# Kernel tuning notes

Measured on AMD Instinct MI355X. Metric: run time of the kernel, lower is better.

The kernel has to match this reference:

```python
import jax, jax.numpy as jnp
import numpy as np

IMAGE_SIZE = 256
NEAR = 0.1
FAR = 100.0
EPS = 1e-3
BACKGROUND = (0.0, 0.0, 0.0)
CHUNK = 64   # faces per scan step (bounds peak memory of the z-buffer pass)
TINY = 1e-12


def _bary(vx, vy, vz, xp, yp):
    """Barycentric weights / perspective-correct depth at pixel centers.
    vx, vy, vz: 3-tuples of vertex coords, broadcastable with xp/yp.
    Mirrors the CUDA kernel: unnormalized cross-product weights, normalize,
    clamp to [0,1], renormalize, zp = 1 / sum(w_k / z_k), near/far clip."""
    x0, x1, x2 = vx; y0, y1, y2 = vy; z0, z1, z2 = vz
    w0 = yp * (x2 - x1) + xp * (y1 - y2) + (x1 * y2 - x2 * y1)
    w1 = yp * (x0 - x2) + xp * (y2 - y0) + (x2 * y0 - x0 * y2)
    w2 = yp * (x1 - x0) + xp * (y0 - y1) + (x0 * y1 - x1 * y0)
    det = w0 + w1 + w2
    safe_det = jnp.where(jnp.abs(det) > TINY, det, 1.0)
    n0, n1, n2 = w0 / safe_det, w1 / safe_det, w2 / safe_det
    inside = (n0 > 0) & (n1 > 0) & (n2 > 0) & (jnp.abs(det) > TINY)
    n0 = jnp.clip(n0, 0.0, 1.0); n1 = jnp.clip(n1, 0.0, 1.0); n2 = jnp.clip(n2, 0.0, 1.0)
    s = n0 + n1 + n2
    s = jnp.where(s > TINY, s, 1.0)
    n0, n1, n2 = n0 / s, n1 / s, n2 / s
    inv_zp = n0 / z0 + n1 / z1 + n2 / z2
    inv_zp = jnp.where(jnp.abs(inv_zp) > TINY, inv_zp, 1.0)
    zp = 1.0 / inv_zp
    valid = inside & (zp > NEAR) & (zp < FAR)
    return (n0, n1, n2), zp, valid


def _pixel_coords():
    IS = IMAGE_SIZE
    return (2.0 * jnp.arange(IS, dtype=jnp.float32) + 1.0 - IS) / IS


def _forward(faces, textures):
    B, F = faces.shape[:2]
    IS = IMAGE_SIZE
    ii = _pixel_coords()

    # ---- pass 1: z-buffer (face-index argmin), chunked scan over faces ----
    # index selection is non-differentiable -> stop_gradient keeps vjp cheap
    fsg = jax.lax.stop_gradient(faces)
    n_chunks = F // CHUNK
    fchunks = jnp.transpose(fsg.reshape(B, n_chunks, CHUNK, 3, 3), (1, 0, 2, 3, 4))
    bases = jnp.arange(n_chunks, dtype=jnp.int32) * CHUNK
    xp4 = ii[None, None, None, :]
    yp4 = ii[None, None, :, None]

    def step(carry, inp):
        depth, fidx = carry
        fc, base = inp                               # fc: [B, CHUNK, 3, 3]
        vx = tuple(fc[:, :, k, 0][:, :, None, None] for k in range(3))
        vy = tuple(fc[:, :, k, 1][:, :, None, None] for k in range(3))
        vz = tuple(fc[:, :, k, 2][:, :, None, None] for k in range(3))
        _, zp, valid = _bary(vx, vy, vz, xp4, yp4)   # [B, CHUNK, IS, IS]
        zp = jnp.where(valid, zp, jnp.inf)
        local = jnp.argmin(zp, axis=1).astype(jnp.int32)
        zbest = jnp.min(zp, axis=1)
        better = zbest < depth
        depth = jnp.where(better, zbest, depth)
        fidx = jnp.where(better, base + local, fidx)
        return (depth, fidx), None

    init = (jnp.full((B, IS, IS), FAR, jnp.float32),
            jnp.full((B, IS, IS), -1, jnp.int32))
    (_, fidx), _ = jax.lax.scan(step, init, (fchunks, bases))

    # ---- pass 2: differentiable recompute for winning faces ----
    mask = fidx >= 0
    safe_idx = jnp.maximum(fidx, 0)
    fsel = jnp.take_along_axis(
        faces.reshape(B, F, 9), safe_idx.reshape(B, -1, 1), axis=1
    ).reshape(B, IS, IS, 3, 3)
    vx = tuple(fsel[..., k, 0] for k in range(3))
    vy = tuple(fsel[..., k, 1] for k in range(3))
    vz = tuple(fsel[..., k, 2] for k in range(3))
    w, zp, _ = _bary(vx, vy, vz, ii[None, None, :], ii[None, :, None])
    depth_map = jnp.where(mask, zp, FAR)

    # ---- texture sampling: 8-corner trilinear in the T^3 face texel cube ----
    T = textures.shape[2]
    tif = [jnp.clip(w[k] * (T - 1) * zp / vz[k], 0.0, T - 1 - EPS) for k in range(3)]
    lo = [jnp.floor(t) for t in tif]
    fr = [t - l for t, l in zip(tif, lo)]
    lo = [l.astype(jnp.int32) for l in lo]

    tex_flat = textures.reshape(B, F * T * T * T, 3)
    base_idx = safe_idx * (T * T * T)
    rgb = jnp.zeros((B, IS, IS, 3), faces.dtype)
    for d0 in (0, 1):
        for d1 in (0, 1):
            for d2 in (0, 1):
                wgt = ((fr[0] if d0 else 1.0 - fr[0]) *
                       (fr[1] if d1 else 1.0 - fr[1]) *
                       (fr[2] if d2 else 1.0 - fr[2]))
                idx = base_idx + (lo[0] + d0) * T * T + (lo[1] + d1) * T + (lo[2] + d2)
                smp = jnp.take_along_axis(tex_flat, idx.reshape(B, -1, 1), axis=1)
                rgb = rgb + wgt[..., None] * smp.reshape(B, IS, IS, 3)

    bg = jnp.asarray(BACKGROUND, faces.dtype)
    mf = mask.astype(faces.dtype)[..., None]
    rgb_map = rgb * mf + (1.0 - mf) * bg
    alpha_map = mask.astype(faces.dtype)
    # pack (rgb, alpha, depth) into a single [B, IS, IS, 5] tensor
    return jnp.concatenate([rgb_map, alpha_map[..., None], depth_map[..., None]], axis=-1)


def setup_inputs() -> dict:
    key = jax.random.key(0)
    B, F, T = 4, 4096, 4
    k1, k2, k3, k4, k5 = jax.random.split(key, 5)
    # small triangles scattered over the screen with depths in (near, far)
    ctr = jax.random.uniform(k1, (B, F, 1, 2), minval=-0.95, maxval=0.95)
    off = jax.random.uniform(k2, (B, F, 3, 2), minval=-0.08, maxval=0.08)
    xy = ctr + off
    zc = jax.random.uniform(k3, (B, F, 1, 1), minval=1.0, maxval=50.0)
    zo = jax.random.uniform(k4, (B, F, 3, 1), minval=-0.2, maxval=0.2)
    faces = jnp.concatenate([xy, zc + zo], axis=-1).astype(jnp.float32)
    textures = jax.random.uniform(k5, (B, F, T, T, T, 3), dtype=jnp.float32)
    return {"faces": faces, "textures": textures}


def reference(faces, textures):
    return _forward(faces, textures)
```

## Files before the change

### kernel.cpp

```cpp
#include <hip/hip_runtime.h>

#define IS 256
#define FCOUNT 4096
#define NEARP 0.1f
#define FARP 100.0f
#define TINYF 1e-12f
#define CAP 256
#define GCAP 128
#define DET_GLOBAL 1e-5f

__device__ __forceinline__ float frn(float r) { asm("" : "+v"(r)); return r; }
__device__ __forceinline__ float mulrn(float a, float b) { return frn(a * b); }
__device__ __forceinline__ float addrn(float a, float b) { return frn(a + b); }
__device__ __forceinline__ float subrn(float a, float b) { return frn(a - b); }
__device__ __forceinline__ float divrn(float a, float b) { return frn(a / b); }
__device__ __forceinline__ float fmarn(float a, float b, float c) {
    return frn(__builtin_fmaf(a, b, c));
}

__global__ __launch_bounds__(256) void bin_kernel(
    const float* __restrict__ faces,
    float4* __restrict__ cA, float4* __restrict__ cB, float4* __restrict__ cC,
    int* __restrict__ counts, int* __restrict__ lists,
    int* __restrict__ gcount, int* __restrict__ glist, int B, int F)
{
    const int gid = blockIdx.x * 256 + threadIdx.x;
    if (gid >= B * F) return;
    const int b = gid >> 12, f = gid & (FCOUNT - 1);
    const float* fp = faces + (size_t)gid * 9;
    const float x0 = fp[0], y0 = fp[1], z0 = fp[2];
    const float x1 = fp[3], y1 = fp[4], z1 = fp[5];
    const float x2 = fp[6], y2 = fp[7], z2 = fp[8];

    const float A0 = subrn(x2, x1), B0 = subrn(y1, y2);
    const float C0 = fmarn(x1, y2, -mulrn(x2, y1));
    const float A1 = subrn(x0, x2), B1 = subrn(y2, y0);
    const float C1 = fmarn(x2, y0, -mulrn(x0, y2));
    const float A2 = subrn(x1, x0), B2 = subrn(y0, y1);
    const float C2 = fmarn(x0, y1, -mulrn(x1, y0));
    cA[gid] = make_float4(A0, B0, C0, A1);
    cB[gid] = make_float4(B1, C1, A2, B2);
    cC[gid] = make_float4(C2, z0, z1, z2);

    const float det = (x1 - x0) * (y2 - y0) - (x2 - x0) * (y1 - y0);
    const float ad = fabsf(det);
    if (ad < DET_GLOBAL) {
        const int pos = atomicAdd(&gcount[b], 1);
        if (pos < GCAP) glist[b * GCAP + pos] = f;
        return;
    }
    const float d = 2e-3f + 3e-7f / ad;
    const float lox = fminf(x0, fminf(x1, x2)) - d;
    const float hix = fmaxf(x0, fmaxf(x1, x2)) + d;
    const float loy = fminf(y0, fminf(y1, y2)) - d;
    const float hiy = fmaxf(y0, fmaxf(y1, y2)) + d;
    int tx0 = (int)floorf((256.f * lox + 255.f) * (1.f / 32.f));
    int tx1 = (int)floorf((256.f * hix + 255.f) * (1.f / 32.f));
    int ty0 = (int)floorf((256.f * loy + 255.f) * (1.f / 32.f));
    int ty1 = (int)floorf((256.f * hiy + 255.f) * (1.f / 32.f));
    tx0 = max(tx0, 0); tx1 = min(tx1, 15);
    ty0 = max(ty0, 0); ty1 = min(ty1, 15);
    for (int ty = ty0; ty <= ty1; ++ty)
        for (int tx = tx0; tx <= tx1; ++tx) {
            const int t = (b * 16 + ty) * 16 + tx;
            const int pos = atomicAdd(&counts[t], 1);
            if (pos < CAP) lists[(size_t)t * CAP + pos] = f;
        }
}

__global__ __launch_bounds__(256) void raster_kernel(
    const float* __restrict__ faces,
    const float* __restrict__ textures,
    const float4* __restrict__ cA, const float4* __restrict__ cB,
    const float4* __restrict__ cC,
    const int* __restrict__ counts, const int* __restrict__ lists,
    const int* __restrict__ gcount, const int* __restrict__ glist,
    float* __restrict__ out, int B, int F)
{
    const int tid  = threadIdx.x;
    const int b    = blockIdx.x >> 8;
    const int tile = blockIdx.x & 255;
    const int px   = (tile & 15) * 16 + (tid & 15);
    const int py   = (tile >> 4) * 16 + (tid >> 4);
    const float xp = (float)(2 * px + 1 - IS) * (1.0f / IS);
    const float yp = (float)(2 * py + 1 - IS) * (1.0f / IS);

    float bestz = FARP;
    int   besti = -1;

    const int cnt  = min(counts[blockIdx.x], CAP);
    const int gcnt = min(gcount[b], GCAP);
    const int total = cnt + gcnt;
    const int* mylist = lists + (size_t)blockIdx.x * CAP;
    const int* gl     = glist + b * GCAP;
    const int fb = b * F;

    for (int j = 0; j < total; ++j) {
        const int fid = (j < cnt) ? mylist[j] : gl[j - cnt];
        const int f = __builtin_amdgcn_readfirstlane(fid);
        const float4 fa = cA[fb + f];
        const float4 fb4 = cB[fb + f];
        const float4 fc = cC[fb + f];
        const float w0 = addrn(fmarn(yp, fa.x, mulrn(xp, fa.y)), fa.z);
        const float w1 = addrn(fmarn(yp, fa.w, mulrn(xp, fb4.x)), fb4.y);
        const float w2 = addrn(fmarn(yp, fb4.z, mulrn(xp, fb4.w)), fc.x);
        const float det = addrn(addrn(w0, w1), w2);
        bool ins;
        if (det > TINYF)       ins = (w0 > 0.f) && (w1 > 0.f) && (w2 > 0.f);
        else if (det < -TINYF) ins = (w0 < 0.f) && (w1 < 0.f) && (w2 < 0.f);
        else                   ins = false;
        if (ins) {
            float n0 = divrn(w0, det), n1 = divrn(w1, det), n2 = divrn(w2, det);
            n0 = frn(fminf(fmaxf(n0, 0.f), 1.f));
            n1 = frn(fminf(fmaxf(n1, 0.f), 1.f));
            n2 = frn(fminf(fmaxf(n2, 0.f), 1.f));
            float s = addrn(addrn(n0, n1), n2);
            s = (s > TINYF) ? s : 1.0f;
            n0 = divrn(n0, s); n1 = divrn(n1, s); n2 = divrn(n2, s);
            float iz = addrn(addrn(divrn(n0, fc.y), divrn(n1, fc.z)),
                             divrn(n2, fc.w));
            iz = (fabsf(iz) > TINYF) ? iz : 1.0f;
            const float zp = divrn(1.0f, iz);
            if (zp > NEARP && zp < FARP) {
                if (zp < bestz || (zp == bestz && f < besti)) {
                    bestz = zp;
                    besti = f;
                }
            }
        }
    }

    const float* fbase = faces + (size_t)b * F * 9;
    float r = 0.f, g = 0.f, bch = 0.f, alpha = 0.f, depth = FARP;
    if (besti >= 0) {
        const float* fp = fbase + (size_t)besti * 9;
        const float x0 = fp[0], y0 = fp[1], z0 = fp[2];
        const float x1 = fp[3], y1 = fp[4], z1 = fp[5];
        const float x2 = fp[6], y2 = fp[7], z2 = fp[8];
        const float w0 = addrn(fmarn(yp, subrn(x2, x1), mulrn(xp, subrn(y1, y2))),
                               fmarn(x1, y2, -mulrn(x2, y1)));
        const float w1 = addrn(fmarn(yp, subrn(x0, x2), mulrn(xp, subrn(y2, y0))),
                               fmarn(x2, y0, -mulrn(x0, y2)));
        const float w2 = addrn(fmarn(yp, subrn(x1, x0), mulrn(xp, subrn(y0, y1))),
                               fmarn(x0, y1, -mulrn(x1, y0)));
        const float det = addrn(addrn(w0, w1), w2);
        const float sd = (fabsf(det) > TINYF) ? det : 1.0f;
        float n0 = divrn(w0, sd), n1 = divrn(w1, sd), n2 = divrn(w2, sd);
        n0 = frn(fminf(fmaxf(n0, 0.f), 1.f));
        n1 = frn(fminf(fmaxf(n1, 0.f), 1.f));
        n2 = frn(fminf(fmaxf(n2, 0.f), 1.f));
        float s = addrn(addrn(n0, n1), n2);
        s = (s > TINYF) ? s : 1.0f;
        n0 = divrn(n0, s); n1 = divrn(n1, s); n2 = divrn(n2, s);
        float iz = addrn(addrn(divrn(n0, z0), divrn(n1, z1)), divrn(n2, z2));
        iz = (fabsf(iz) > TINYF) ? iz : 1.0f;
        const float zp = divrn(1.0f, iz);
        depth = zp;

        const float t0 = fminf(fmaxf(divrn(mulrn(mulrn(n0, 3.0f), zp), z0), 0.f), 2.999f);
        const float t1 = fminf(fmaxf(divrn(mulrn(mulrn(n1, 3.0f), zp), z1), 0.f), 2.999f);
        const float t2 = fminf(fmaxf(divrn(mulrn(mulrn(n2, 3.0f), zp), z2), 0.f), 2.999f);
        const float l0 = floorf(t0), l1 = floorf(t1), l2 = floorf(t2);
        const float fr0 = subrn(t0, l0), fr1 = subrn(t1, l1), fr2 = subrn(t2, l2);
        const int i0 = (int)l0, i1 = (int)l1, i2 = (int)l2;

        const float* tx = textures + (size_t)(b * F + besti) * 64 * 3;
        for (int d0 = 0; d0 < 2; ++d0)
            for (int d1 = 0; d1 < 2; ++d1)
                for (int d2 = 0; d2 < 2; ++d2) {
                    const float wg = mulrn(mulrn(d0 ? fr0 : subrn(1.0f, fr0),
                                                 d1 ? fr1 : subrn(1.0f, fr1)),
                                           d2 ? fr2 : subrn(1.0f, fr2));
                    const float* tp = tx + ((i0 + d0) * 16 + (i1 + d1) * 4 + (i2 + d2)) * 3;
                    r   = addrn(r,   mulrn(wg, tp[0]));
                    g   = addrn(g,   mulrn(wg, tp[1]));
                    bch = addrn(bch, mulrn(wg, tp[2]));
                }
        alpha = 1.0f;
    }

    float* op = out + (((size_t)b * IS + py) * IS + px) * 5;
    op[0] = r;
    op[1] = g;
    op[2] = bch;
    op[3] = alpha;
    op[4] = depth;
}

extern "C" void kernel_launch(void* const* d_in, const int* in_sizes, int n_in,
                              void* d_out, int out_size, void* d_ws, size_t ws_size,
                              hipStream_t stream) {
    const float* faces    = (const float*)d_in[0];
    const float* textures = (const float*)d_in[1];
    float* out = (float*)d_out;
    const int F = FCOUNT;
    const int B = in_sizes[0] / (F * 9);
    const int ntiles = B * 256;

    int* counts = (int*)d_ws;
    int* gcount = counts + ntiles;
    int* glist  = gcount + B;
    int* lists  = glist + B * GCAP;
    float4* cA  = (float4*)(lists + (size_t)ntiles * CAP);
    float4* cB  = cA + (size_t)B * F;
    float4* cC  = cB + (size_t)B * F;

    hipMemsetAsync(counts, 0, (size_t)(ntiles + B) * sizeof(int), stream);
    bin_kernel<<<dim3((B * F + 255) / 256), dim3(256), 0, stream>>>(
        faces, cA, cB, cC, counts, lists, gcount, glist, B, F);
    raster_kernel<<<dim3(ntiles), dim3(256), 0, stream>>>(
        faces, textures, cA, cB, cC, counts, lists, gcount, glist, out, B, F);
}
```

Baseline: 117.1 us.

## Stage per-tile face coefficients in shared memory; shrink bin kernel blocks

The raster loop now loads up to 256 face coefficient records cooperatively into LDS, one per thread, and each thread then reads them from shared memory. Before, every wave fetched cA/cB/cC from global memory for each face in sequence. This is meant to cut serialized global-load latency in the inner loop, at the cost of two block barriers per batch. The bin kernel also switches to 64-thread blocks, giving more, smaller blocks.

Result: faster. 109.1 us (-6.8%).

```diff
diff --git a/kernel.cpp b/kernel.cpp
--- a/kernel.cpp
+++ b/kernel.cpp
@@ -18,13 +18,13 @@
     return frn(__builtin_fmaf(a, b, c));
 }
 
-__global__ __launch_bounds__(256) void bin_kernel(
+__global__ __launch_bounds__(64) void bin_kernel(
     const float* __restrict__ faces,
     float4* __restrict__ cA, float4* __restrict__ cB, float4* __restrict__ cC,
     int* __restrict__ counts, int* __restrict__ lists,
     int* __restrict__ gcount, int* __restrict__ glist, int B, int F)
 {
-    const int gid = blockIdx.x * 256 + threadIdx.x;
+    const int gid = blockIdx.x * 64 + threadIdx.x;
     if (gid >= B * F) return;
     const int b = gid >> 12, f = gid & (FCOUNT - 1);
     const float* fp = faces + (size_t)gid * 9;
@@ -85,6 +85,11 @@
     const float xp = (float)(2 * px + 1 - IS) * (1.0f / IS);
     const float yp = (float)(2 * py + 1 - IS) * (1.0f / IS);
 
+    __shared__ float4 s_a[256];
+    __shared__ float4 s_b[256];
+    __shared__ float4 s_c[256];
+    __shared__ int    s_idx[256];
+
     float bestz = FARP;
     int   besti = -1;
 
@@ -95,39 +100,52 @@
     const int* gl     = glist + b * GCAP;
     const int fb = b * F;
 
-    for (int j = 0; j < total; ++j) {
-        const int fid = (j < cnt) ? mylist[j] : gl[j - cnt];
-        const int f = __builtin_amdgcn_readfirstlane(fid);
-        const float4 fa = cA[fb + f];
-        const float4 fb4 = cB[fb + f];
-        const float4 fc = cC[fb + f];
-        const float w0 = addrn(fmarn(yp, fa.x, mulrn(xp, fa.y)), fa.z);
-        const float w1 = addrn(fmarn(yp, fa.w, mulrn(xp, fb4.x)), fb4.y);
-        const float w2 = addrn(fmarn(yp, fb4.z, mulrn(xp, fb4.w)), fc.x);
-        const float det = addrn(addrn(w0, w1), w2);
-        bool ins;
-        if (det > TINYF)       ins = (w0 > 0.f) && (w1 > 0.f) && (w2 > 0.f);
-        else if (det < -TINYF) ins = (w0 < 0.f) && (w1 < 0.f) && (w2 < 0.f);
-        else                   ins = false;
-        if (ins) {
-            float n0 = divrn(w0, det), n1 = divrn(w1, det), n2 = divrn(w2, det);
-            n0 = frn(fminf(fmaxf(n0, 0.f), 1.f));
-            n1 = frn(fminf(fmaxf(n1, 0.f), 1.f));
-            n2 = frn(fminf(fmaxf(n2, 0.f), 1.f));
-            float s = addrn(addrn(n0, n1), n2);
-            s = (s > TINYF) ? s : 1.0f;
-            n0 = divrn(n0, s); n1 = divrn(n1, s); n2 = divrn(n2, s);
-            float iz = addrn(addrn(divrn(n0, fc.y), divrn(n1, fc.z)),
-                             divrn(n2, fc.w));
-            iz = (fabsf(iz) > TINYF) ? iz : 1.0f;
-            const float zp = divrn(1.0f, iz);
-            if (zp > NEARP && zp < FARP) {
-                if (zp < bestz || (zp == bestz && f < besti)) {
-                    bestz = zp;
-                    besti = f;
+    for (int cbase = 0; cbase < total; cbase += 256) {
+        const int m = min(total - cbase, 256);
+        if (tid < m) {
+            const int k = cbase + tid;
+            const int f = (k < cnt) ? mylist[k] : gl[k - cnt];
+            s_a[tid] = cA[fb + f];
+            s_b[tid] = cB[fb + f];
+            s_c[tid] = cC[fb + f];
+            s_idx[tid] = f;
+        }
+        __syncthreads();
+
+        for (int j = 0; j < m; ++j) {
+            const float4 fa = s_a[j];
+            const float4 fb4 = s_b[j];
+            const float4 fc = s_c[j];
+            const float w0 = addrn(fmarn(yp, fa.x, mulrn(xp, fa.y)), fa.z);
+            const float w1 = addrn(fmarn(yp, fa.w, mulrn(xp, fb4.x)), fb4.y);
+            const float w2 = addrn(fmarn(yp, fb4.z, mulrn(xp, fb4.w)), fc.x);
+            const float det = addrn(addrn(w0, w1), w2);
+            bool ins;
+            if (det > TINYF)       ins = (w0 > 0.f) && (w1 > 0.f) && (w2 > 0.f);
+            else if (det < -TINYF) ins = (w0 < 0.f) && (w1 < 0.f) && (w2 < 0.f);
+            else                   ins = false;
+            if (ins) {
+                float n0 = divrn(w0, det), n1 = divrn(w1, det), n2 = divrn(w2, det);
+                n0 = frn(fminf(fmaxf(n0, 0.f), 1.f));
+                n1 = frn(fminf(fmaxf(n1, 0.f), 1.f));
+                n2 = frn(fminf(fmaxf(n2, 0.f), 1.f));
+                float s = addrn(addrn(n0, n1), n2);
+                s = (s > TINYF) ? s : 1.0f;
+                n0 = divrn(n0, s); n1 = divrn(n1, s); n2 = divrn(n2, s);
+                float iz = addrn(addrn(divrn(n0, fc.y), divrn(n1, fc.z)),
+                                 divrn(n2, fc.w));
+                iz = (fabsf(iz) > TINYF) ? iz : 1.0f;
+                const float zp = divrn(1.0f, iz);
+                if (zp > NEARP && zp < FARP) {
+                    const int fi = s_idx[j];
+                    if (zp < bestz || (zp == bestz && fi < besti)) {
+                        bestz = zp;
+                        besti = fi;
+                    }
                 }
             }
         }
+        __syncthreads();
     }
 
     const float* fbase = faces + (size_t)b * F * 9;
@@ -206,7 +224,7 @@
     float4* cC  = cB + (size_t)B * F;
 
     hipMemsetAsync(counts, 0, (size_t)(ntiles + B) * sizeof(int), stream);
-    bin_kernel<<<dim3((B * F + 255) / 256), dim3(256), 0, stream>>>(
+    bin_kernel<<<dim3((B * F + 63) / 64), dim3(64), 0, stream>>>(
         faces, cA, cB, cC, counts, lists, gcount, glist, B, F);
     raster_kernel<<<dim3(ntiles), dim3(256), 0, stream>>>(
         faces, textures, cA, cB, cC, counts, lists, gcount, glist, out, B, F);
```
